# Optimization experiments

Hardware: AMD Instinct MI355X
Metric: run time of the kernel (lower is better)

## Reference

```python
import jax, jax.numpy as jnp
import numpy as np

D_MODEL = 1024
NUM_HEADS = 16
D_K = D_MODEL // NUM_HEADS


def setup_inputs() -> dict:
    key = jax.random.key(0)
    ks = jax.random.split(key, 11)
    B, S = 2, 2048
    s = 1.0 / np.sqrt(D_MODEL)
    inp = {
        'Q': jax.random.normal(ks[0], (B, S, D_MODEL), jnp.float32),
        'K': jax.random.normal(ks[1], (B, S, D_MODEL), jnp.float32),
        'V': jax.random.normal(ks[2], (B, S, D_MODEL), jnp.float32),
        'Wq': jax.random.normal(ks[3], (D_MODEL, D_MODEL), jnp.float32) * s,
        'bq': jnp.zeros((D_MODEL,), jnp.float32),
        'Wk': jax.random.normal(ks[4], (D_MODEL, D_MODEL), jnp.float32) * s,
        'bk': jnp.zeros((D_MODEL,), jnp.float32),
        'Wv': jax.random.normal(ks[5], (D_MODEL, D_MODEL), jnp.float32) * s,
        'bv': jnp.zeros((D_MODEL,), jnp.float32),
        'Wo': jax.random.normal(ks[6], (D_MODEL, D_MODEL), jnp.float32) * s,
        'bo': jnp.zeros((D_MODEL,), jnp.float32),
    }
    return inp


def _split_heads(x, B):
    # [B, S, D] -> [B, H, S, d_k]
    return x.reshape(B, -1, NUM_HEADS, D_K).transpose(0, 2, 1, 3)


def reference(Q, K, V, Wq, bq, Wk, bk, Wv, bv, Wo, bo):
    B, S, _ = Q.shape
    q = _split_heads(Q @ Wq.T + bq, B)  # [B,H,S,dk]
    k = _split_heads(K @ Wk.T + bk, B)
    v = _split_heads(V @ Wv.T + bv, B)
    scale = 1.0 / jnp.sqrt(jnp.asarray(D_K, q.dtype))
    scores = jnp.einsum('bhqd,bhkd->bhqk', q, k) * scale  # full [B,H,S,S] (naive)
    attn = jax.nn.softmax(scores, axis=-1)
    ctx = jnp.einsum('bhqk,bhkd->bhqd', attn, v)
    ctx = ctx.transpose(0, 2, 1, 3).reshape(B, S, D_MODEL)
    out = ctx @ Wo.T + bo  # dropout in eval mode = identity
    return out
```

## Files before the change

### kernel.cpp

```cpp
#include <hip/hip_runtime.h>
#include <hip/hip_bf16.h>


typedef __attribute__((ext_vector_type(8))) short short8;
typedef __attribute__((ext_vector_type(4))) float f32x4;
typedef __attribute__((ext_vector_type(4))) unsigned short us4;

static constexpr int D_MODEL = 1024;
static constexpr int NHEAD   = 16;
static constexpr int DK      = 64;
static constexpr int SEQ     = 2048;
static constexpr int BATCH   = 2;
static constexpr int MTOT    = BATCH * SEQ;

#define DEVINL __device__ __forceinline__

DEVINL unsigned short f2bf(float f) {
    __hip_bfloat16 h = __float2bfloat16(f);
    return *reinterpret_cast<unsigned short*>(&h);
}

__global__ __launch_bounds__(256) void cast_f32_bf16(
    const float* __restrict__ s0, const float* __restrict__ s1,
    const float* __restrict__ s2, const float* __restrict__ s3,
    unsigned short* __restrict__ d0, unsigned short* __restrict__ d1,
    unsigned short* __restrict__ d2, unsigned short* __restrict__ d3,
    int n)
{
    const float* s; unsigned short* d;
    switch (blockIdx.y) {
        case 0:  s = s0; d = d0; break;
        case 1:  s = s1; d = d1; break;
        case 2:  s = s2; d = d2; break;
        default: s = s3; d = d3; break;
    }
    int i = (blockIdx.x * 256 + threadIdx.x) * 8;
    if (i + 8 > n) return;
    float4 v0 = *reinterpret_cast<const float4*>(s + i);
    float4 v1 = *reinterpret_cast<const float4*>(s + i + 4);
    union { unsigned short u[8]; short8 v; } o;
    o.u[0] = f2bf(v0.x); o.u[1] = f2bf(v0.y); o.u[2] = f2bf(v0.z); o.u[3] = f2bf(v0.w);
    o.u[4] = f2bf(v1.x); o.u[5] = f2bf(v1.y); o.u[6] = f2bf(v1.z); o.u[7] = f2bf(v1.w);
    *reinterpret_cast<short8*>(d + i) = o.v;
}

template<int MODE>
DEVINL void gemm_core(const unsigned short* __restrict__ A,
                      const unsigned short* __restrict__ W,
                      const float* __restrict__ bias,
                      void* __restrict__ outp,
                      int m0, int n0,
                      unsigned short* a_lds, unsigned short* b_lds)
{
    constexpr int K = 1024;
    const int tid  = threadIdx.x;
    const int wave = tid >> 6, lane = tid & 63;
    const int wrow = (wave >> 1) * 64, wcol = (wave & 1) * 64;
    const int fr = lane & 15, fg = lane >> 4;

    f32x4 acc[4][4];
    #pragma unroll
    for (int i = 0; i < 4; ++i)
        #pragma unroll
        for (int j = 0; j < 4; ++j)
            acc[i][j] = (f32x4){0.f, 0.f, 0.f, 0.f};

    const int c0 = tid, c1 = tid + 256;
    const unsigned short* gA0 = A + (size_t)(m0 + (c0 >> 2)) * K + (c0 & 3) * 8;
    const unsigned short* gA1 = A + (size_t)(m0 + (c1 >> 2)) * K + (c1 & 3) * 8;
    const unsigned short* gB0 = W + (size_t)(n0 + (c0 >> 2)) * K + (c0 & 3) * 8;
    const unsigned short* gB1 = W + (size_t)(n0 + (c1 >> 2)) * K + (c1 & 3) * 8;
    char* aLb = (char*)a_lds + wave * 1024;
    char* bLb = (char*)b_lds + wave * 1024;

    const unsigned short* aF = a_lds + (wrow + fr) * 32 + fg * 8;
    const unsigned short* bF = b_lds + (wcol + fr) * 32 + fg * 8;

    for (int kt = 0; kt < K / 32; ++kt) {
        __syncthreads();
        __builtin_amdgcn_global_load_lds(gA0 + kt * 32, aLb,        16, 0, 0);
        __builtin_amdgcn_global_load_lds(gA1 + kt * 32, aLb + 4096, 16, 0, 0);
        __builtin_amdgcn_global_load_lds(gB0 + kt * 32, bLb,        16, 0, 0);
        __builtin_amdgcn_global_load_lds(gB1 + kt * 32, bLb + 4096, 16, 0, 0);
        __syncthreads();

        short8 af[4], bf[4];
        #pragma unroll
        for (int mt = 0; mt < 4; ++mt)
            af[mt] = *reinterpret_cast<const short8*>(aF + mt * 16 * 32);
        #pragma unroll
        for (int nt = 0; nt < 4; ++nt)
            bf[nt] = *reinterpret_cast<const short8*>(bF + nt * 16 * 32);
        #pragma unroll
        for (int mt = 0; mt < 4; ++mt)
            #pragma unroll
            for (int nt = 0; nt < 4; ++nt)
                acc[mt][nt] = __builtin_amdgcn_mfma_f32_16x16x32_bf16(
                    af[mt], bf[nt], acc[mt][nt], 0, 0, 0);
    }

    #pragma unroll
    for (int mt = 0; mt < 4; ++mt) {
        #pragma unroll
        for (int nt = 0; nt < 4; ++nt) {
            f32x4 v = acc[mt][nt];
            const int n = n0 + wcol + nt * 16 + fr;
            const float bi = bias[n];
            if constexpr (MODE == 2) {
                #pragma unroll
                for (int r = 0; r < 4; ++r) {
                    const int m = m0 + wrow + mt * 16 + fg * 4 + r;
                    ((float*)outp)[(size_t)m * D_MODEL + n] = v[r] + bi;
                }
            } else if constexpr (MODE == 0) {
                #pragma unroll
                for (int r = 0; r < 4; ++r) {
                    const int m = m0 + wrow + mt * 16 + fg * 4 + r;
                    const int b = m >> 11, s = m & 2047;
                    const int h = n >> 6,  d = n & 63;
                    ((unsigned short*)outp)[((size_t)(b * NHEAD + h) * SEQ + s) * DK + d]
                        = f2bf(v[r] + bi);
                }
            } else {
                const int sbase = m0 + wrow + mt * 16 + fg * 4;
                const int b = sbase >> 11, s = sbase & 2047;
                const int h = n >> 6, d = n & 63;
                us4 pk;
                #pragma unroll
                for (int r = 0; r < 4; ++r)
                    pk[r] = f2bf(v[r] + bi);
                *reinterpret_cast<us4*>(
                    (unsigned short*)outp
                    + ((size_t)(b * NHEAD + h) * DK + d) * SEQ + s) = pk;
            }
        }
    }
}

__global__ __launch_bounds__(256) void qkv_gemm(
    const unsigned short* __restrict__ Qb, const unsigned short* __restrict__ Kb,
    const unsigned short* __restrict__ Vb,
    const unsigned short* __restrict__ Wq, const unsigned short* __restrict__ Wk,
    const unsigned short* __restrict__ Wv,
    const float* __restrict__ bq, const float* __restrict__ bk,
    const float* __restrict__ bv,
    unsigned short* __restrict__ qh, unsigned short* __restrict__ kh,
    unsigned short* __restrict__ vT)
{
    __shared__ unsigned short a_lds[128 * 32];
    __shared__ unsigned short b_lds[128 * 32];
    const int sel = blockIdx.y >> 3;
    const int n0  = (blockIdx.y & 7) * 128;
    const int m0  = blockIdx.x * 128;
    if (sel == 0)      gemm_core<0>(Qb, Wq, bq, qh, m0, n0, a_lds, b_lds);
    else if (sel == 1) gemm_core<0>(Kb, Wk, bk, kh, m0, n0, a_lds, b_lds);
    else               gemm_core<1>(Vb, Wv, bv, vT, m0, n0, a_lds, b_lds);
}

__global__ __launch_bounds__(256) void oproj_gemm(
    const unsigned short* __restrict__ ctx, const unsigned short* __restrict__ Wo,
    const float* __restrict__ bo, float* __restrict__ out)
{
    __shared__ unsigned short a_lds[128 * 32];
    __shared__ unsigned short b_lds[128 * 32];
    gemm_core<2>(ctx, Wo, bo, out, blockIdx.x * 128, blockIdx.y * 128, a_lds, b_lds);
}

__global__ __launch_bounds__(256) void attn_fwd(
    const unsigned short* __restrict__ qh,
    const unsigned short* __restrict__ kh,
    const unsigned short* __restrict__ vT,
    unsigned short* __restrict__ ctx)
{
    __shared__ unsigned short k_lds[64 * 64];
    __shared__ unsigned short v_lds[64 * 64];
    __shared__ unsigned short p_lds[4][16 * 64];

    const int tid  = threadIdx.x;
    const int wave = tid >> 6, lane = tid & 63;
    const int fr = lane & 15, fg = lane >> 4;
    const int swz = (fr & 7) << 4;
    const int h = blockIdx.y, b = blockIdx.z;
    const int q0 = blockIdx.x * 64 + wave * 16;

    const size_t headoff = (size_t)(b * NHEAD + h) * SEQ * DK;
    const unsigned short* qbase = qh + headoff;
    const unsigned short* kbase = kh + headoff;
    const unsigned short* vbase = vT + headoff;

    short8 qf[2];
    #pragma unroll
    for (int ks = 0; ks < 2; ++ks)
        qf[ks] = *reinterpret_cast<const short8*>(
            qbase + (size_t)(q0 + fr) * DK + ks * 32 + fg * 8);

    const int c0 = tid, c1 = 256 + tid;
    const int r0 = c0 >> 3, s0 = (c0 & 7) ^ (r0 & 7);
    const int r1 = c1 >> 3, s1 = (c1 & 7) ^ (r1 & 7);
    const unsigned short* gk0 = kbase + (size_t)r0 * DK + s0 * 8;
    const unsigned short* gk1 = kbase + (size_t)r1 * DK + s1 * 8;
    const unsigned short* gv0 = vbase + (size_t)r0 * SEQ + s0 * 8;
    const unsigned short* gv1 = vbase + (size_t)r1 * SEQ + s1 * 8;
    char* kl0 = (char*)k_lds + wave * 1024;
    char* kl1 = (char*)k_lds + 4096 + wave * 1024;
    char* vl0 = (char*)v_lds + wave * 1024;
    char* vl1 = (char*)v_lds + 4096 + wave * 1024;
    char* pwr = (char*)p_lds[wave];
    const char* prd = (const char*)p_lds[wave] + fr * 128;

    f32x4 oacc[4];
    #pragma unroll
    for (int i = 0; i < 4; ++i) oacc[i] = (f32x4){0.f, 0.f, 0.f, 0.f};
    float mrun[4], lpart[4];
    #pragma unroll
    for (int r = 0; r < 4; ++r) { mrun[r] = -1e30f; lpart[r] = 0.f; }

    constexpr float SCL = 0.125f * 1.44269504088896340736f;
    constexpr float THR = 8.0f;

    for (int kt = 0; kt < SEQ / 64; ++kt) {
        const int kv0 = kt * 64;
        __syncthreads();
        __builtin_amdgcn_global_load_lds(gk0 + (size_t)kv0 * DK, kl0, 16, 0, 0);
        __builtin_amdgcn_global_load_lds(gk1 + (size_t)kv0 * DK, kl1, 16, 0, 0);
        __builtin_amdgcn_global_load_lds(gv0 + kv0,              vl0, 16, 0, 0);
        __builtin_amdgcn_global_load_lds(gv1 + kv0,              vl1, 16, 0, 0);
        __syncthreads();

        f32x4 sacc[4];
        #pragma unroll
        for (int i = 0; i < 4; ++i) sacc[i] = (f32x4){0.f, 0.f, 0.f, 0.f};
        #pragma unroll
        for (int ks = 0; ks < 2; ++ks) {
            #pragma unroll
            for (int nt = 0; nt < 4; ++nt) {
                const int krow = nt * 16 + fr;
                short8 kf = *reinterpret_cast<const short8*>(
                    (const char*)k_lds + krow * 128 + ((ks * 64 + fg * 16) ^ swz));
                sacc[nt] = __builtin_amdgcn_mfma_f32_16x16x32_bf16(
                    qf[ks], kf, sacc[nt], 0, 0, 0);
            }
        }

        #pragma unroll
        for (int nt = 0; nt < 4; ++nt)
            #pragma unroll
            for (int r = 0; r < 4; ++r)
                sacc[nt][r] *= SCL;

        float lmax[4];
        bool need = false;
        #pragma unroll
        for (int r = 0; r < 4; ++r) {
            lmax[r] = fmaxf(fmaxf(sacc[0][r], sacc[1][r]),
                            fmaxf(sacc[2][r], sacc[3][r]));
            need |= (lmax[r] > mrun[r] + THR);
        }
        if (__any(need)) {
            #pragma unroll
            for (int r = 0; r < 4; ++r) {
                float mx = fmaxf(lmax[r], mrun[r]);
                mx = fmaxf(mx, __shfl_xor(mx, 1));
                mx = fmaxf(mx, __shfl_xor(mx, 2));
                mx = fmaxf(mx, __shfl_xor(mx, 4));
                mx = fmaxf(mx, __shfl_xor(mx, 8));
                const float alpha = __builtin_amdgcn_exp2f(mrun[r] - mx);
                mrun[r] = mx;
                lpart[r] *= alpha;
                #pragma unroll
                for (int ntd = 0; ntd < 4; ++ntd)
                    oacc[ntd][r] *= alpha;
            }
        }

        #pragma unroll
        for (int r = 0; r < 4; ++r) {
            float rs = 0.f;
            #pragma unroll
            for (int nt = 0; nt < 4; ++nt) {
                const float p = __builtin_amdgcn_exp2f(sacc[nt][r] - mrun[r]);
                sacc[nt][r] = p;
                rs += p;
            }
            lpart[r] += rs;
        }

        #pragma unroll
        for (int nt = 0; nt < 4; ++nt)
            #pragma unroll
            for (int r = 0; r < 4; ++r) {
                const int qrow = fg * 4 + r;
                *(unsigned short*)(pwr + qrow * 128
                    + ((nt * 32 + fr * 2) ^ ((qrow & 7) << 4)))
                    = f2bf(sacc[nt][r]);
            }

        #pragma unroll
        for (int ks = 0; ks < 2; ++ks) {
            short8 pf = *reinterpret_cast<const short8*>(
                prd + ((ks * 64 + fg * 16) ^ swz));
            #pragma unroll
            for (int ntd = 0; ntd < 4; ++ntd) {
                const int vrow = ntd * 16 + fr;
                short8 vf = *reinterpret_cast<const short8*>(
                    (const char*)v_lds + vrow * 128 + ((ks * 64 + fg * 16) ^ swz));
                oacc[ntd] = __builtin_amdgcn_mfma_f32_16x16x32_bf16(
                    pf, vf, oacc[ntd], 0, 0, 0);
            }
        }
    }

    float inv[4];
    #pragma unroll
    for (int r = 0; r < 4; ++r) {
        float s = lpart[r];
        s += __shfl_xor(s, 1);
        s += __shfl_xor(s, 2);
        s += __shfl_xor(s, 4);
        s += __shfl_xor(s, 8);
        inv[r] = 1.f / s;
    }
    #pragma unroll
    for (int ntd = 0; ntd < 4; ++ntd)
        #pragma unroll
        for (int r = 0; r < 4; ++r) {
            const int qg = q0 + fg * 4 + r;
            const size_t off = ((size_t)(b * SEQ + qg)) * D_MODEL
                             + h * DK + ntd * 16 + fr;
            ctx[off] = f2bf(oacc[ntd][r] * inv[r]);
        }
}

extern "C" void kernel_launch(void* const* d_in, const int* in_sizes, int n_in,
                              void* d_out, int out_size, void* d_ws, size_t ws_size,
                              hipStream_t stream)
{
    const float* Q  = (const float*)d_in[0];
    const float* K  = (const float*)d_in[1];
    const float* V  = (const float*)d_in[2];
    const float* Wq = (const float*)d_in[3];
    const float* bq = (const float*)d_in[4];
    const float* Wk = (const float*)d_in[5];
    const float* bk = (const float*)d_in[6];
    const float* Wv = (const float*)d_in[7];
    const float* bv = (const float*)d_in[8];
    const float* Wo = (const float*)d_in[9];
    const float* bo = (const float*)d_in[10];

    char* ws = (char*)d_ws;
    const size_t SZ_ACT = (size_t)MTOT * D_MODEL * 2;
    const size_t SZ_W   = (size_t)D_MODEL * D_MODEL * 2;
    unsigned short* Qb  = (unsigned short*)(ws);
    unsigned short* Kb  = (unsigned short*)(ws + SZ_ACT);
    unsigned short* Vb  = (unsigned short*)(ws + 2 * SZ_ACT);
    unsigned short* Wqb = (unsigned short*)(ws + 3 * SZ_ACT);
    unsigned short* Wkb = (unsigned short*)(ws + 3 * SZ_ACT + SZ_W);
    unsigned short* Wvb = (unsigned short*)(ws + 3 * SZ_ACT + 2 * SZ_W);
    unsigned short* Wob = (unsigned short*)(ws + 3 * SZ_ACT + 3 * SZ_W);
    unsigned short* qhd = (unsigned short*)(ws + 3 * SZ_ACT + 4 * SZ_W);
    unsigned short* khd = (unsigned short*)(ws + 4 * SZ_ACT + 4 * SZ_W);
    unsigned short* vTd = (unsigned short*)(ws + 5 * SZ_ACT + 4 * SZ_W);
    unsigned short* ctx = (unsigned short*)(ws + 6 * SZ_ACT + 4 * SZ_W);

    const int nAct = MTOT * D_MODEL;
    const int nW   = D_MODEL * D_MODEL;

    cast_f32_bf16<<<dim3(nAct / (256 * 8), 3), 256, 0, stream>>>(
        Q, K, V, nullptr, Qb, Kb, Vb, nullptr, nAct);
    cast_f32_bf16<<<dim3(nW / (256 * 8), 4), 256, 0, stream>>>(
        Wq, Wk, Wv, Wo, Wqb, Wkb, Wvb, Wob, nW);

    qkv_gemm<<<dim3(MTOT / 128, 24), 256, 0, stream>>>(
        Qb, Kb, Vb, Wqb, Wkb, Wvb, bq, bk, bv, qhd, khd, vTd);

    attn_fwd<<<dim3(SEQ / 64, NHEAD, BATCH), 256, 0, stream>>>(
        qhd, khd, vTd, ctx);

    oproj_gemm<<<dim3(MTOT / 128, D_MODEL / 128), 256, 0, stream>>>(
        ctx, Wob, bo, (float*)d_out);
}
```

Before: 249.8 us.

## Double-buffer LDS tiles in GEMMs and attention; fold softmax scale into Q projection

Both the GEMM core and the attention kernel now use two LDS buffers, issuing the async global-to-LDS loads for the next tile before computing on the current one, with one barrier per iteration instead of two. The softmax scale (1/sqrt(dk)*log2e) is folded into the Q projection epilogue, removing a per-tile multiply in attention. MFMA sections are wrapped in s_setprio raises. The extra LDS doubles per-block shared memory, which may reduce occupancy, and Q is now rounded to bf16 after scaling.

Measured after the change: 249.3 us. About the same (-0.2%).

```diff
diff --git a/kernel.cpp b/kernel.cpp
--- a/kernel.cpp
+++ b/kernel.cpp
@@ -12,6 +12,8 @@
 static constexpr int SEQ     = 2048;
 static constexpr int BATCH   = 2;
 static constexpr int MTOT    = BATCH * SEQ;
+
+static constexpr float QSCL = 0.125f * 1.44269504088896340736f;
 
 #define DEVINL __device__ __forceinline__
 
@@ -49,7 +51,7 @@
                       const unsigned short* __restrict__ W,
                       const float* __restrict__ bias,
                       void* __restrict__ outp,
-                      int m0, int n0,
+                      int m0, int n0, float oscale,
                       unsigned short* a_lds, unsigned short* b_lds)
 {
     constexpr int K = 1024;
@@ -73,17 +75,23 @@
     char* aLb = (char*)a_lds + wave * 1024;
     char* bLb = (char*)b_lds + wave * 1024;
 
-    const unsigned short* aF = a_lds + (wrow + fr) * 32 + fg * 8;
-    const unsigned short* bF = b_lds + (wcol + fr) * 32 + fg * 8;
+    auto stage = [&](int buf, int kt) {
+        const int bo = buf * 8192;
+        __builtin_amdgcn_global_load_lds(gA0 + kt * 32, aLb + bo,        16, 0, 0);
+        __builtin_amdgcn_global_load_lds(gA1 + kt * 32, aLb + bo + 4096, 16, 0, 0);
+        __builtin_amdgcn_global_load_lds(gB0 + kt * 32, bLb + bo,        16, 0, 0);
+        __builtin_amdgcn_global_load_lds(gB1 + kt * 32, bLb + bo + 4096, 16, 0, 0);
+    };
+
+    stage(0, 0);
+    __syncthreads();
+    int cur = 0;
 
     for (int kt = 0; kt < K / 32; ++kt) {
-        __syncthreads();
-        __builtin_amdgcn_global_load_lds(gA0 + kt * 32, aLb,        16, 0, 0);
-        __builtin_amdgcn_global_load_lds(gA1 + kt * 32, aLb + 4096, 16, 0, 0);
-        __builtin_amdgcn_global_load_lds(gB0 + kt * 32, bLb,        16, 0, 0);
-        __builtin_amdgcn_global_load_lds(gB1 + kt * 32, bLb + 4096, 16, 0, 0);
-        __syncthreads();
-
+        if (kt + 1 < K / 32) stage(cur ^ 1, kt + 1);
+
+        const unsigned short* aF = a_lds + cur * 4096 + (wrow + fr) * 32 + fg * 8;
+        const unsigned short* bF = b_lds + cur * 4096 + (wcol + fr) * 32 + fg * 8;
         short8 af[4], bf[4];
         #pragma unroll
         for (int mt = 0; mt < 4; ++mt)
@@ -91,12 +99,17 @@
         #pragma unroll
         for (int nt = 0; nt < 4; ++nt)
             bf[nt] = *reinterpret_cast<const short8*>(bF + nt * 16 * 32);
+        __builtin_amdgcn_s_setprio(1);
         #pragma unroll
         for (int mt = 0; mt < 4; ++mt)
             #pragma unroll
             for (int nt = 0; nt < 4; ++nt)
                 acc[mt][nt] = __builtin_amdgcn_mfma_f32_16x16x32_bf16(
                     af[mt], bf[nt], acc[mt][nt], 0, 0, 0);
+        __builtin_amdgcn_s_setprio(0);
+
+        __syncthreads();
+        cur ^= 1;
     }
 
     #pragma unroll
@@ -110,7 +123,7 @@
                 #pragma unroll
                 for (int r = 0; r < 4; ++r) {
                     const int m = m0 + wrow + mt * 16 + fg * 4 + r;
-                    ((float*)outp)[(size_t)m * D_MODEL + n] = v[r] + bi;
+                    ((float*)outp)[(size_t)m * D_MODEL + n] = (v[r] + bi) * oscale;
                 }
             } else if constexpr (MODE == 0) {
                 #pragma unroll
@@ -119,7 +132,7 @@
                     const int b = m >> 11, s = m & 2047;
                     const int h = n >> 6,  d = n & 63;
                     ((unsigned short*)outp)[((size_t)(b * NHEAD + h) * SEQ + s) * DK + d]
-                        = f2bf(v[r] + bi);
+                        = f2bf((v[r] + bi) * oscale);
                 }
             } else {
                 const int sbase = m0 + wrow + mt * 16 + fg * 4;
@@ -128,7 +141,7 @@
                 us4 pk;
                 #pragma unroll
                 for (int r = 0; r < 4; ++r)
-                    pk[r] = f2bf(v[r] + bi);
+                    pk[r] = f2bf((v[r] + bi) * oscale);
                 *reinterpret_cast<us4*>(
                     (unsigned short*)outp
                     + ((size_t)(b * NHEAD + h) * DK + d) * SEQ + s) = pk;
@@ -147,23 +160,24 @@
     unsigned short* __restrict__ qh, unsigned short* __restrict__ kh,
     unsigned short* __restrict__ vT)
 {
-    __shared__ unsigned short a_lds[128 * 32];
-    __shared__ unsigned short b_lds[128 * 32];
+    __shared__ unsigned short a_lds[2 * 128 * 32];
+    __shared__ unsigned short b_lds[2 * 128 * 32];
     const int sel = blockIdx.y >> 3;
     const int n0  = (blockIdx.y & 7) * 128;
     const int m0  = blockIdx.x * 128;
-    if (sel == 0)      gemm_core<0>(Qb, Wq, bq, qh, m0, n0, a_lds, b_lds);
-    else if (sel == 1) gemm_core<0>(Kb, Wk, bk, kh, m0, n0, a_lds, b_lds);
-    else               gemm_core<1>(Vb, Wv, bv, vT, m0, n0, a_lds, b_lds);
+    if (sel == 0)      gemm_core<0>(Qb, Wq, bq, qh, m0, n0, QSCL, a_lds, b_lds);
+    else if (sel == 1) gemm_core<0>(Kb, Wk, bk, kh, m0, n0, 1.0f, a_lds, b_lds);
+    else               gemm_core<1>(Vb, Wv, bv, vT, m0, n0, 1.0f, a_lds, b_lds);
 }
 
 __global__ __launch_bounds__(256) void oproj_gemm(
     const unsigned short* __restrict__ ctx, const unsigned short* __restrict__ Wo,
     const float* __restrict__ bo, float* __restrict__ out)
 {
-    __shared__ unsigned short a_lds[128 * 32];
-    __shared__ unsigned short b_lds[128 * 32];
-    gemm_core<2>(ctx, Wo, bo, out, blockIdx.x * 128, blockIdx.y * 128, a_lds, b_lds);
+    __shared__ unsigned short a_lds[2 * 128 * 32];
+    __shared__ unsigned short b_lds[2 * 128 * 32];
+    gemm_core<2>(ctx, Wo, bo, out, blockIdx.x * 128, blockIdx.y * 128, 1.0f,
+                 a_lds, b_lds);
 }
 
 __global__ __launch_bounds__(256) void attn_fwd(
@@ -172,8 +186,8 @@
     const unsigned short* __restrict__ vT,
     unsigned short* __restrict__ ctx)
 {
-    __shared__ unsigned short k_lds[64 * 64];
-    __shared__ unsigned short v_lds[64 * 64];
+    __shared__ unsigned short k_lds[2][64 * 64];
+    __shared__ unsigned short v_lds[2][64 * 64];
     __shared__ unsigned short p_lds[4][16 * 64];
 
     const int tid  = threadIdx.x;
@@ -195,58 +209,60 @@
             qbase + (size_t)(q0 + fr) * DK + ks * 32 + fg * 8);
 
     const int c0 = tid, c1 = 256 + tid;
-    const int r0 = c0 >> 3, s0 = (c0 & 7) ^ (r0 & 7);
-    const int r1 = c1 >> 3, s1 = (c1 & 7) ^ (r1 & 7);
-    const unsigned short* gk0 = kbase + (size_t)r0 * DK + s0 * 8;
-    const unsigned short* gk1 = kbase + (size_t)r1 * DK + s1 * 8;
-    const unsigned short* gv0 = vbase + (size_t)r0 * SEQ + s0 * 8;
-    const unsigned short* gv1 = vbase + (size_t)r1 * SEQ + s1 * 8;
-    char* kl0 = (char*)k_lds + wave * 1024;
-    char* kl1 = (char*)k_lds + 4096 + wave * 1024;
-    char* vl0 = (char*)v_lds + wave * 1024;
-    char* vl1 = (char*)v_lds + 4096 + wave * 1024;
+    const int r0 = c0 >> 3, s0i = (c0 & 7) ^ (r0 & 7);
+    const int r1 = c1 >> 3, s1i = (c1 & 7) ^ (r1 & 7);
+    const unsigned short* gk0 = kbase + (size_t)r0 * DK + s0i * 8;
+    const unsigned short* gk1 = kbase + (size_t)r1 * DK + s1i * 8;
+    const unsigned short* gv0 = vbase + (size_t)r0 * SEQ + s0i * 8;
+    const unsigned short* gv1 = vbase + (size_t)r1 * SEQ + s1i * 8;
+
+    auto stage = [&](int buf, int kv0) {
+        char* kb = (char*)k_lds[buf] + wave * 1024;
+        char* vb = (char*)v_lds[buf] + wave * 1024;
+        __builtin_amdgcn_global_load_lds(gk0 + (size_t)kv0 * DK, kb,        16, 0, 0);
+        __builtin_amdgcn_global_load_lds(gk1 + (size_t)kv0 * DK, kb + 4096, 16, 0, 0);
+        __builtin_amdgcn_global_load_lds(gv0 + kv0,              vb,        16, 0, 0);
+        __builtin_amdgcn_global_load_lds(gv1 + kv0,              vb + 4096, 16, 0, 0);
+    };
+
+    f32x4 oacc[4];
+    #pragma unroll
+    for (int i = 0; i < 4; ++i) oacc[i] = (f32x4){0.f, 0.f, 0.f, 0.f};
+    float mrun[4], lpart[4];
+    #pragma unroll
+    for (int r = 0; r < 4; ++r) { mrun[r] = -1e30f; lpart[r] = 0.f; }
+
+    constexpr float THR = 8.0f;
+
     char* pwr = (char*)p_lds[wave];
     const char* prd = (const char*)p_lds[wave] + fr * 128;
 
-    f32x4 oacc[4];
-    #pragma unroll
-    for (int i = 0; i < 4; ++i) oacc[i] = (f32x4){0.f, 0.f, 0.f, 0.f};
-    float mrun[4], lpart[4];
-    #pragma unroll
-    for (int r = 0; r < 4; ++r) { mrun[r] = -1e30f; lpart[r] = 0.f; }
-
-    constexpr float SCL = 0.125f * 1.44269504088896340736f;
-    constexpr float THR = 8.0f;
+    stage(0, 0);
+    __syncthreads();
+    int cur = 0;
 
     for (int kt = 0; kt < SEQ / 64; ++kt) {
-        const int kv0 = kt * 64;
-        __syncthreads();
-        __builtin_amdgcn_global_load_lds(gk0 + (size_t)kv0 * DK, kl0, 16, 0, 0);
-        __builtin_amdgcn_global_load_lds(gk1 + (size_t)kv0 * DK, kl1, 16, 0, 0);
-        __builtin_amdgcn_global_load_lds(gv0 + kv0,              vl0, 16, 0, 0);
-        __builtin_amdgcn_global_load_lds(gv1 + kv0,              vl1, 16, 0, 0);
-        __syncthreads();
+        if (kt + 1 < SEQ / 64) stage(cur ^ 1, (kt + 1) * 64);
+
+        const char* kl = (const char*)k_lds[cur];
+        const char* vl = (const char*)v_lds[cur];
 
         f32x4 sacc[4];
         #pragma unroll
         for (int i = 0; i < 4; ++i) sacc[i] = (f32x4){0.f, 0.f, 0.f, 0.f};
+        __builtin_amdgcn_s_setprio(1);
         #pragma unroll
         for (int ks = 0; ks < 2; ++ks) {
             #pragma unroll
             for (int nt = 0; nt < 4; ++nt) {
                 const int krow = nt * 16 + fr;
                 short8 kf = *reinterpret_cast<const short8*>(
-                    (const char*)k_lds + krow * 128 + ((ks * 64 + fg * 16) ^ swz));
+                    kl + krow * 128 + ((ks * 64 + fg * 16) ^ swz));
                 sacc[nt] = __builtin_amdgcn_mfma_f32_16x16x32_bf16(
                     qf[ks], kf, sacc[nt], 0, 0, 0);
             }
         }
-
-        #pragma unroll
-        for (int nt = 0; nt < 4; ++nt)
-            #pragma unroll
-            for (int r = 0; r < 4; ++r)
-                sacc[nt][r] *= SCL;
+        __builtin_amdgcn_s_setprio(0);
 
         float lmax[4];
         bool need = false;
@@ -299,15 +315,20 @@
         for (int ks = 0; ks < 2; ++ks) {
             short8 pf = *reinterpret_cast<const short8*>(
                 prd + ((ks * 64 + fg * 16) ^ swz));
+            __builtin_amdgcn_s_setprio(1);
             #pragma unroll
             for (int ntd = 0; ntd < 4; ++ntd) {
                 const int vrow = ntd * 16 + fr;
                 short8 vf = *reinterpret_cast<const short8*>(
-                    (const char*)v_lds + vrow * 128 + ((ks * 64 + fg * 16) ^ swz));
+                    vl + vrow * 128 + ((ks * 64 + fg * 16) ^ swz));
                 oacc[ntd] = __builtin_amdgcn_mfma_f32_16x16x32_bf16(
                     pf, vf, oacc[ntd], 0, 0, 0);
             }
-        }
+            __builtin_amdgcn_s_setprio(0);
+        }
+
+        __syncthreads();
+        cur ^= 1;
     }
 
     float inv[4];
```
